# Kernel optimization log

Measured on AMD Instinct MI355X. Metric: run time of the kernel, lower is better.

The kernel has to match this reference:

```python
import jax, jax.numpy as jnp
import numpy as np

N = 50000      # nodes
E = 800000     # edges (avg degree 16)
IN = 256       # in_dim
OUT = 128      # out_dim
H = 4          # heads
D = OUT // H   # head_dim = 32


def setup_inputs() -> dict:
    key = jax.random.key(0)
    k1, k2, k3, k4 = jax.random.split(key, 4)
    x = jax.random.normal(k1, (N, IN), dtype=jnp.float32)
    edge_index = jax.random.randint(k2, (2, E), 0, N, dtype=jnp.int32)
    W = jax.random.normal(k3, (OUT, IN), dtype=jnp.float32) * 0.05   # Linear(in_dim, out_dim, bias=False)
    a_w = jax.random.normal(k4, (2 * D,), dtype=jnp.float32) * 0.05  # Linear(2*head_dim, 1, bias=False)
    return {"x": x, "edge_index": edge_index, "W": W, "a_w": a_w}


def reference(x, edge_index, W, a_w):
    # Wx: [N, H, D]
    Wx = (x @ W.T).reshape(N, H, D)
    src, dst = edge_index[0], edge_index[1]
    # a([Wx_src, Wx_dst]) == Wx_src @ a_w[:D] + Wx_dst @ a_w[D:]; compute per-node then gather
    a_s, a_d = a_w[:D], a_w[D:]
    s_src = jnp.einsum('nhd,d->nh', Wx, a_s)  # [N, H]
    s_dst = jnp.einsum('nhd,d->nh', Wx, a_d)  # [N, H]
    e = jax.nn.leaky_relu(s_src[src] + s_dst[dst], negative_slope=0.2)  # [E, H]
    e_exp = jnp.exp(e)
    denom = jax.ops.segment_sum(e_exp, dst, num_segments=N)             # [N, H]
    alpha = e_exp / (denom[dst] + 1e-8)                                 # [E, H] (dropout=0 / eval)
    weighted = alpha[..., None] * Wx[src]                               # [E, H, D]
    out = jax.ops.segment_sum(weighted, dst, num_segments=N)            # [N, H, D]
    return jax.nn.elu(out.reshape(N, OUT))
```

## Files before the change

### kernel.cpp

```cpp
#include <hip/hip_runtime.h>
#include <math.h>

#define NN 50000
#define NE 800000
#define INF_ 256
#define OUTF 128
#define CAPB 64
#define PB 0xAAAAAAAAu

#define GBM 64
#define GEMM_BLOCKS ((NN + GBM - 1) / GBM)
#define SCAT_BLOCKS (NE / 256)
#define XLD 40

typedef __attribute__((ext_vector_type(8))) __bf16 bf16x8;
typedef __attribute__((ext_vector_type(8))) unsigned short ushort8;
typedef __attribute__((ext_vector_type(4))) float floatx4;

__device__ __forceinline__ unsigned short f2bf(float v) {
    unsigned int u = __float_as_uint(v);
    return (unsigned short)((u + 0x7FFFu + ((u >> 16) & 1u)) >> 16);
}
__device__ __forceinline__ float bf2f(unsigned short u) {
    return __uint_as_float(((unsigned int)u) << 16);
}
__device__ __forceinline__ void split8(const float4& a, const float4& b,
                                       bf16x8& hi, bf16x8& lo) {
    const float v[8] = {a.x, a.y, a.z, a.w, b.x, b.y, b.z, b.w};
    ushort8 h, l;
#pragma unroll
    for (int i = 0; i < 8; ++i) {
        unsigned short hb = f2bf(v[i]);
        h[i] = hb;
        l[i] = f2bf(v[i] - bf2f(hb));
    }
    hi = __builtin_bit_cast(bf16x8, h);
    lo = __builtin_bit_cast(bf16x8, l);
}

__global__ __launch_bounds__(256) void gemm_scatter_kernel(
    const float* __restrict__ x, const float* __restrict__ W,
    const float* __restrict__ a_w, unsigned short* __restrict__ Wxh,
    float* __restrict__ s_src, float* __restrict__ s_dst,
    const int* __restrict__ src, const int* __restrict__ dst,
    int* __restrict__ fill, unsigned short* __restrict__ colsrc)
{
    __shared__ __align__(16) unsigned short xhi[GBM * XLD];
    __shared__ __align__(16) unsigned short xlo[GBM * XLD];
    const int t = threadIdx.x;

    if (blockIdx.x >= GEMM_BLOCKS) {
        int i = (blockIdx.x - GEMM_BLOCKS) * 256 + t;
        int d = dst[i];
        unsigned pos = (unsigned)atomicAdd(&fill[d], 1) - PB;
        if (pos < CAPB) colsrc[d * CAPB + pos] = (unsigned short)src[i];
        return;
    }

    const int w = t >> 6, lane = t & 63;
    const int g = lane >> 4, il = lane & 15;
    const int bm = blockIdx.x * GBM;
    const int cb = w * 32;

    floatx4 acc[4][2];
#pragma unroll
    for (int mt = 0; mt < 4; ++mt)
#pragma unroll
        for (int nt = 0; nt < 2; ++nt)
            acc[mt][nt] = (floatx4){0.f, 0.f, 0.f, 0.f};

    for (int kc = 0; kc < INF_; kc += 32) {
#pragma unroll
        for (int p = 0; p < 2; ++p) {
            int f = t + p * 256;
            int row = f >> 3, kq = (f & 7) * 4;
            int gr = bm + row;
            float4 v = make_float4(0.f, 0.f, 0.f, 0.f);
            if (gr < NN) v = *(const float4*)&x[(size_t)gr * INF_ + kc + kq];
            ushort4 hv, lv;
            hv.x = f2bf(v.x); lv.x = f2bf(v.x - bf2f(hv.x));
            hv.y = f2bf(v.y); lv.y = f2bf(v.y - bf2f(hv.y));
            hv.z = f2bf(v.z); lv.z = f2bf(v.z - bf2f(hv.z));
            hv.w = f2bf(v.w); lv.w = f2bf(v.w - bf2f(hv.w));
            *(ushort4*)&xhi[row * XLD + kq] = hv;
            *(ushort4*)&xlo[row * XLD + kq] = lv;
        }
        __syncthreads();

        bf16x8 Bh[2], Bl[2];
#pragma unroll
        for (int nt = 0; nt < 2; ++nt) {
            const float* wp = &W[(size_t)(cb + nt * 16 + il) * INF_ + kc + g * 8];
            float4 v0 = *(const float4*)wp;
            float4 v1 = *(const float4*)(wp + 4);
            split8(v0, v1, Bh[nt], Bl[nt]);
        }
#pragma unroll
        for (int mt = 0; mt < 4; ++mt) {
            bf16x8 Ah = *(const bf16x8*)&xhi[(mt * 16 + il) * XLD + g * 8];
            bf16x8 Al = *(const bf16x8*)&xlo[(mt * 16 + il) * XLD + g * 8];
            acc[mt][0] = __builtin_amdgcn_mfma_f32_16x16x32_bf16(Ah, Bh[0], acc[mt][0], 0, 0, 0);
            acc[mt][0] = __builtin_amdgcn_mfma_f32_16x16x32_bf16(Al, Bh[0], acc[mt][0], 0, 0, 0);
            acc[mt][0] = __builtin_amdgcn_mfma_f32_16x16x32_bf16(Ah, Bl[0], acc[mt][0], 0, 0, 0);
            acc[mt][1] = __builtin_amdgcn_mfma_f32_16x16x32_bf16(Ah, Bh[1], acc[mt][1], 0, 0, 0);
            acc[mt][1] = __builtin_amdgcn_mfma_f32_16x16x32_bf16(Al, Bh[1], acc[mt][1], 0, 0, 0);
            acc[mt][1] = __builtin_amdgcn_mfma_f32_16x16x32_bf16(Ah, Bl[1], acc[mt][1], 0, 0, 0);
        }
        __syncthreads();
    }

    const float as0 = a_w[il],      as1 = a_w[16 + il];
    const float ad0 = a_w[32 + il], ad1 = a_w[48 + il];
#pragma unroll
    for (int mt = 0; mt < 4; ++mt) {
#pragma unroll
        for (int r = 0; r < 4; ++r) {
            int row = bm + mt * 16 + g * 4 + r;
            float v0 = acc[mt][0][r], v1 = acc[mt][1][r];
            if (row < NN) {
                Wxh[(size_t)row * OUTF + cb + il]      = f2bf(v0);
                Wxh[(size_t)row * OUTF + cb + 16 + il] = f2bf(v1);
            }
            float ps = v0 * as0 + v1 * as1;
            float pd = v0 * ad0 + v1 * ad1;
            ps += __shfl_xor(ps, 1); ps += __shfl_xor(ps, 2);
            ps += __shfl_xor(ps, 4); ps += __shfl_xor(ps, 8);
            pd += __shfl_xor(pd, 1); pd += __shfl_xor(pd, 2);
            pd += __shfl_xor(pd, 4); pd += __shfl_xor(pd, 8);
            if (il == 0 && row < NN) {
                s_src[row * 4 + w] = ps;
                s_dst[row * 4 + w] = pd;
            }
        }
    }
}

__global__ __launch_bounds__(256) void gat_out_kernel(
    const unsigned short* __restrict__ Wxh, const float* __restrict__ s_src,
    const float* __restrict__ s_dst, const int* __restrict__ fill,
    const unsigned short* __restrict__ colsrc, float* __restrict__ out)
{
    __shared__ float lexp[4][CAPB * 4];
    __shared__ int   lsrc[4][CAPB];
    const int w = threadIdx.x >> 6;
    const int lane = threadIdx.x & 63;
    const int wid = (blockIdx.x << 2) + w;
    const unsigned dr = (unsigned)fill[wid] - PB;
    const int deg = dr < CAPB ? (int)dr : CAPB;
    const float4 sd = *(const float4*)&s_dst[(size_t)wid * 4];

    float e0 = 0.f, e1 = 0.f, e2 = 0.f, e3 = 0.f;
    int s = 0;
    if (lane < deg) {
        s = colsrc[wid * CAPB + lane];
        float4 ss = *(const float4*)&s_src[(size_t)s * 4];
        float t0 = ss.x + sd.x; t0 = t0 > 0.f ? t0 : 0.2f * t0; e0 = expf(t0);
        float t1 = ss.y + sd.y; t1 = t1 > 0.f ? t1 : 0.2f * t1; e1 = expf(t1);
        float t2 = ss.z + sd.z; t2 = t2 > 0.f ? t2 : 0.2f * t2; e2 = expf(t2);
        float t3 = ss.w + sd.w; t3 = t3 > 0.f ? t3 : 0.2f * t3; e3 = expf(t3);
    }
    float d0 = e0, d1 = e1, d2 = e2, d3 = e3;
#pragma unroll
    for (int o = 32; o > 0; o >>= 1) {
        d0 += __shfl_xor(d0, o);
        d1 += __shfl_xor(d1, o);
        d2 += __shfl_xor(d2, o);
        d3 += __shfl_xor(d3, o);
    }
    const float i0 = 1.f / (d0 + 1e-8f), i1 = 1.f / (d1 + 1e-8f);
    const float i2 = 1.f / (d2 + 1e-8f), i3 = 1.f / (d3 + 1e-8f);
    *(float4*)&lexp[w][lane * 4] = make_float4(e0 * i0, e1 * i1, e2 * i2, e3 * i3);
    lsrc[w][lane] = (lane < deg) ? (s << 8) : 0;
    __syncthreads();

    const int el = lane >> 5;
    const int fl = lane & 31;
    const int f = fl * 4;
    const int h = fl >> 3;
    const char* wbase = (const char*)Wxh + f * 2;

    float a0 = 0.f, a1 = 0.f, a2 = 0.f, a3 = 0.f;
    float b0 = 0.f, b1 = 0.f, b2 = 0.f, b3 = 0.f;
    for (int q = 0; q < deg; q += 4) {
        int o0 = lsrc[w][q + el];
        int o1 = lsrc[w][q + 2 + el];
        float al0 = lexp[w][(q + el) * 4 + h];
        float al1 = lexp[w][(q + 2 + el) * 4 + h];
        ushort4 u0 = *(const ushort4*)(wbase + o0);
        ushort4 u1 = *(const ushort4*)(wbase + o1);
        a0 = fmaf(al0, bf2f(u0.x), a0); a1 = fmaf(al0, bf2f(u0.y), a1);
        a2 = fmaf(al0, bf2f(u0.z), a2); a3 = fmaf(al0, bf2f(u0.w), a3);
        b0 = fmaf(al1, bf2f(u1.x), b0); b1 = fmaf(al1, bf2f(u1.y), b1);
        b2 = fmaf(al1, bf2f(u1.z), b2); b3 = fmaf(al1, bf2f(u1.w), b3);
    }
    a0 += b0; a1 += b1; a2 += b2; a3 += b3;
    a0 += __shfl_xor(a0, 32); a1 += __shfl_xor(a1, 32);
    a2 += __shfl_xor(a2, 32); a3 += __shfl_xor(a3, 32);
    if (el == 0) {
        a0 = a0 > 0.f ? a0 : expm1f(a0);
        a1 = a1 > 0.f ? a1 : expm1f(a1);
        a2 = a2 > 0.f ? a2 : expm1f(a2);
        a3 = a3 > 0.f ? a3 : expm1f(a3);
        *(float4*)&out[(size_t)wid * OUTF + f] = make_float4(a0, a1, a2, a3);
    }
}

extern "C" void kernel_launch(void* const* d_in, const int* in_sizes, int n_in,
                              void* d_out, int out_size, void* d_ws, size_t ws_size,
                              hipStream_t stream) {
    const float* x   = (const float*)d_in[0];
    const int*   ei  = (const int*)d_in[1];
    const float* W   = (const float*)d_in[2];
    const float* a_w = (const float*)d_in[3];
    const int* esrc = ei;
    const int* edst = ei + NE;
    float* out = (float*)d_out;

    char* ws = (char*)d_ws;
    size_t off = 0;
    auto alloc = [&](size_t bytes) -> char* {
        char* p = ws + off;
        off += (bytes + 255) & ~(size_t)255;
        return p;
    };
    unsigned short* Wxh = (unsigned short*)alloc((size_t)NN * OUTF * 2);
    float* s_src  = (float*)alloc((size_t)NN * 4 * 4);
    float* s_dst  = (float*)alloc((size_t)NN * 4 * 4);
    int*   fill   = (int*)alloc((size_t)NN * 4);
    unsigned short* colsrc = (unsigned short*)alloc((size_t)NN * CAPB * 2);

    gemm_scatter_kernel<<<dim3(GEMM_BLOCKS + SCAT_BLOCKS), dim3(256), 0, stream>>>(
        x, W, a_w, Wxh, s_src, s_dst, esrc, edst, fill, colsrc);
    gat_out_kernel<<<dim3(NN / 4), dim3(256), 0, stream>>>(
        Wxh, s_src, s_dst, fill, colsrc, out);
}
```

Baseline: 185.0 us.

## Fuse GEMM, scatter and aggregation into one cooperative persistent kernel

Merges the GEMM+CSR-scatter kernel and the attention aggregation kernel into a single cooperative launch of 1024 persistent blocks, separated by a grid-wide sync. This removes the second kernel launch and the gap between the two kernels. The aggregation loop also unrolls from 2 to 4 gather streams per lane to put more loads in flight. The cost is that occupancy is capped at the persistent grid size, which may hurt the latency-bound gather phase, and there is a grid barrier; the old two-kernel path is kept as a fallback if the cooperative launch fails.

```diff
diff --git a/kernel.cpp b/kernel.cpp
--- a/kernel.cpp
+++ b/kernel.cpp
@@ -1,5 +1,8 @@
 #include <hip/hip_runtime.h>
+#include <hip/hip_cooperative_groups.h>
 #include <math.h>
+
+namespace cg = cooperative_groups;
 
 #define NN 50000
 #define NE 800000
@@ -11,6 +14,7 @@
 #define GBM 64
 #define GEMM_BLOCKS ((NN + GBM - 1) / GBM)
 #define SCAT_BLOCKS (NE / 256)
+#define GRIDB 1024
 #define XLD 40
 
 typedef __attribute__((ext_vector_type(8))) __bf16 bf16x8;
@@ -38,28 +42,15 @@
     lo = __builtin_bit_cast(bf16x8, l);
 }
 
-__global__ __launch_bounds__(256) void gemm_scatter_kernel(
-    const float* __restrict__ x, const float* __restrict__ W,
+__device__ __forceinline__ void gemm_tile(
+    int bid, int t, const float* __restrict__ x, const float* __restrict__ W,
     const float* __restrict__ a_w, unsigned short* __restrict__ Wxh,
     float* __restrict__ s_src, float* __restrict__ s_dst,
-    const int* __restrict__ src, const int* __restrict__ dst,
-    int* __restrict__ fill, unsigned short* __restrict__ colsrc)
-{
-    __shared__ __align__(16) unsigned short xhi[GBM * XLD];
-    __shared__ __align__(16) unsigned short xlo[GBM * XLD];
-    const int t = threadIdx.x;
-
-    if (blockIdx.x >= GEMM_BLOCKS) {
-        int i = (blockIdx.x - GEMM_BLOCKS) * 256 + t;
-        int d = dst[i];
-        unsigned pos = (unsigned)atomicAdd(&fill[d], 1) - PB;
-        if (pos < CAPB) colsrc[d * CAPB + pos] = (unsigned short)src[i];
-        return;
-    }
-
+    unsigned short* xhi, unsigned short* xlo)
+{
     const int w = t >> 6, lane = t & 63;
     const int g = lane >> 4, il = lane & 15;
-    const int bm = blockIdx.x * GBM;
+    const int bm = bid * GBM;
     const int cb = w * 32;
 
     floatx4 acc[4][2];
@@ -135,16 +126,12 @@
     }
 }
 
-__global__ __launch_bounds__(256) void gat_out_kernel(
-    const unsigned short* __restrict__ Wxh, const float* __restrict__ s_src,
-    const float* __restrict__ s_dst, const int* __restrict__ fill,
-    const unsigned short* __restrict__ colsrc, float* __restrict__ out)
-{
-    __shared__ float lexp[4][CAPB * 4];
-    __shared__ int   lsrc[4][CAPB];
-    const int w = threadIdx.x >> 6;
-    const int lane = threadIdx.x & 63;
-    const int wid = (blockIdx.x << 2) + w;
+__device__ __forceinline__ void gat_node_group(
+    int wid, int w, int lane, const unsigned short* __restrict__ Wxh,
+    const float* __restrict__ s_src, const float* __restrict__ s_dst,
+    const int* __restrict__ fill, const unsigned short* __restrict__ colsrc,
+    float* __restrict__ out, float* lexp, int* lsrc)
+{
     const unsigned dr = (unsigned)fill[wid] - PB;
     const int deg = dr < CAPB ? (int)dr : CAPB;
     const float4 sd = *(const float4*)&s_dst[(size_t)wid * 4];
@@ -169,8 +156,9 @@
     }
     const float i0 = 1.f / (d0 + 1e-8f), i1 = 1.f / (d1 + 1e-8f);
     const float i2 = 1.f / (d2 + 1e-8f), i3 = 1.f / (d3 + 1e-8f);
-    *(float4*)&lexp[w][lane * 4] = make_float4(e0 * i0, e1 * i1, e2 * i2, e3 * i3);
-    lsrc[w][lane] = (lane < deg) ? (s << 8) : 0;
+    *(float4*)&lexp[(w * 64 + lane) * 4] =
+        make_float4(e0 * i0, e1 * i1, e2 * i2, e3 * i3);
+    lsrc[w * 64 + lane] = (lane < deg) ? (s << 8) : 0;
     __syncthreads();
 
     const int el = lane >> 5;
@@ -181,19 +169,32 @@
 
     float a0 = 0.f, a1 = 0.f, a2 = 0.f, a3 = 0.f;
     float b0 = 0.f, b1 = 0.f, b2 = 0.f, b3 = 0.f;
-    for (int q = 0; q < deg; q += 4) {
-        int o0 = lsrc[w][q + el];
-        int o1 = lsrc[w][q + 2 + el];
-        float al0 = lexp[w][(q + el) * 4 + h];
-        float al1 = lexp[w][(q + 2 + el) * 4 + h];
+    float g0 = 0.f, g1 = 0.f, g2 = 0.f, g3 = 0.f;
+    float h0 = 0.f, h1 = 0.f, h2 = 0.f, h3 = 0.f;
+    for (int q = 0; q < deg; q += 8) {
+        int o0 = lsrc[w * 64 + q + el];
+        int o1 = lsrc[w * 64 + q + 2 + el];
+        int o2 = lsrc[w * 64 + q + 4 + el];
+        int o3 = lsrc[w * 64 + q + 6 + el];
+        float al0 = lexp[(w * 64 + q + el) * 4 + h];
+        float al1 = lexp[(w * 64 + q + 2 + el) * 4 + h];
+        float al2 = lexp[(w * 64 + q + 4 + el) * 4 + h];
+        float al3 = lexp[(w * 64 + q + 6 + el) * 4 + h];
         ushort4 u0 = *(const ushort4*)(wbase + o0);
         ushort4 u1 = *(const ushort4*)(wbase + o1);
+        ushort4 u2 = *(const ushort4*)(wbase + o2);
+        ushort4 u3 = *(const ushort4*)(wbase + o3);
         a0 = fmaf(al0, bf2f(u0.x), a0); a1 = fmaf(al0, bf2f(u0.y), a1);
         a2 = fmaf(al0, bf2f(u0.z), a2); a3 = fmaf(al0, bf2f(u0.w), a3);
         b0 = fmaf(al1, bf2f(u1.x), b0); b1 = fmaf(al1, bf2f(u1.y), b1);
         b2 = fmaf(al1, bf2f(u1.z), b2); b3 = fmaf(al1, bf2f(u1.w), b3);
-    }
-    a0 += b0; a1 += b1; a2 += b2; a3 += b3;
+        g0 = fmaf(al2, bf2f(u2.x), g0); g1 = fmaf(al2, bf2f(u2.y), g1);
+        g2 = fmaf(al2, bf2f(u2.z), g2); g3 = fmaf(al2, bf2f(u2.w), g3);
+        h0 = fmaf(al3, bf2f(u3.x), h0); h1 = fmaf(al3, bf2f(u3.y), h1);
+        h2 = fmaf(al3, bf2f(u3.z), h2); h3 = fmaf(al3, bf2f(u3.w), h3);
+    }
+    a0 += b0 + g0 + h0; a1 += b1 + g1 + h1;
+    a2 += b2 + g2 + h2; a3 += b3 + g3 + h3;
     a0 += __shfl_xor(a0, 32); a1 += __shfl_xor(a1, 32);
     a2 += __shfl_xor(a2, 32); a3 += __shfl_xor(a3, 32);
     if (el == 0) {
@@ -203,6 +204,76 @@
         a3 = a3 > 0.f ? a3 : expm1f(a3);
         *(float4*)&out[(size_t)wid * OUTF + f] = make_float4(a0, a1, a2, a3);
     }
+}
+
+__global__ __launch_bounds__(256) void mega_kernel(
+    const float* __restrict__ x, const float* __restrict__ W,
+    const float* __restrict__ a_w, const int* __restrict__ src,
+    const int* __restrict__ dst, unsigned short* __restrict__ Wxh,
+    float* __restrict__ s_src, float* __restrict__ s_dst,
+    int* __restrict__ fill, unsigned short* __restrict__ colsrc,
+    float* __restrict__ out)
+{
+    __shared__ __align__(16) unsigned char smem[10240];
+    const int t = threadIdx.x;
+    const int bid = blockIdx.x;
+    const int w = t >> 6, lane = t & 63;
+
+    if (bid < GEMM_BLOCKS)
+        gemm_tile(bid, t, x, W, a_w, Wxh, s_src, s_dst,
+                  (unsigned short*)smem, (unsigned short*)(smem + 5120));
+
+    for (int e = bid * 256 + t; e < NE; e += GRIDB * 256) {
+        int d = dst[e];
+        unsigned pos = (unsigned)atomicAdd(&fill[d], 1) - PB;
+        if (pos < CAPB) colsrc[d * CAPB + pos] = (unsigned short)src[e];
+    }
+
+    __threadfence();
+    cg::this_grid().sync();
+    __threadfence();
+
+    float* lexp = (float*)smem;
+    int*   lsrc = (int*)(smem + 4096);
+    for (int grp = bid; grp < NN / 4; grp += GRIDB) {
+        gat_node_group((grp << 2) + w, w, lane, Wxh, s_src, s_dst,
+                       fill, colsrc, out, lexp, lsrc);
+        __syncthreads();
+    }
+}
+
+__global__ __launch_bounds__(256) void gemm_scatter_kernel(
+    const float* __restrict__ x, const float* __restrict__ W,
+    const float* __restrict__ a_w, unsigned short* __restrict__ Wxh,
+    float* __restrict__ s_src, float* __restrict__ s_dst,
+    const int* __restrict__ src, const int* __restrict__ dst,
+    int* __restrict__ fill, unsigned short* __restrict__ colsrc)
+{
+    __shared__ __align__(16) unsigned short xhi[GBM * XLD];
+    __shared__ __align__(16) unsigned short xlo[GBM * XLD];
+    const int t = threadIdx.x;
+    if (blockIdx.x >= GEMM_BLOCKS) {
+        int i = (blockIdx.x - GEMM_BLOCKS) * 256 + t;
+        int d = dst[i];
+        unsigned pos = (unsigned)atomicAdd(&fill[d], 1) - PB;
+        if (pos < CAPB) colsrc[d * CAPB + pos] = (unsigned short)src[i];
+        return;
+    }
+    gemm_tile(blockIdx.x, t, x, W, a_w, Wxh, s_src, s_dst, xhi, xlo);
+}
+
+__global__ __launch_bounds__(256) void gat_out_kernel(
+    const unsigned short* __restrict__ Wxh, const float* __restrict__ s_src,
+    const float* __restrict__ s_dst, const int* __restrict__ fill,
+    const unsigned short* __restrict__ colsrc, float* __restrict__ out)
+{
+    __shared__ __align__(16) unsigned char smem[5120];
+    float* lexp = (float*)smem;
+    int*   lsrc = (int*)(smem + 4096);
+    const int w = threadIdx.x >> 6;
+    const int lane = threadIdx.x & 63;
+    gat_node_group((blockIdx.x << 2) + w, w, lane, Wxh, s_src, s_dst,
+                   fill, colsrc, out, lexp, lsrc);
 }
 
 extern "C" void kernel_launch(void* const* d_in, const int* in_sizes, int n_in,
@@ -229,8 +300,16 @@
     int*   fill   = (int*)alloc((size_t)NN * 4);
     unsigned short* colsrc = (unsigned short*)alloc((size_t)NN * CAPB * 2);
 
-    gemm_scatter_kernel<<<dim3(GEMM_BLOCKS + SCAT_BLOCKS), dim3(256), 0, stream>>>(
-        x, W, a_w, Wxh, s_src, s_dst, esrc, edst, fill, colsrc);
-    gat_out_kernel<<<dim3(NN / 4), dim3(256), 0, stream>>>(
-        Wxh, s_src, s_dst, fill, colsrc, out);
-}
+    void* args[] = {(void*)&x, (void*)&W, (void*)&a_w, (void*)&esrc, (void*)&edst,
+                    (void*)&Wxh, (void*)&s_src, (void*)&s_dst, (void*)&fill,
+                    (void*)&colsrc, (void*)&out};
+    hipError_t err = hipLaunchCooperativeKernel((const void*)mega_kernel,
+                                                dim3(GRIDB), dim3(256),
+                                                args, 0, stream);
+    if (err != hipSuccess) {
+        gemm_scatter_kernel<<<dim3(GEMM_BLOCKS + SCAT_BLOCKS), dim3(256), 0, stream>>>(
+            x, W, a_w, Wxh, s_src, s_dst, esrc, edst, fill, colsrc);
+        gat_out_kernel<<<dim3(NN / 4), dim3(256), 0, stream>>>(
+            Wxh, s_src, s_dst, fill, colsrc, out);
+    }
+}
```

New measurement: 526.6 us. +184.7%, slower.
